# Kernel tuning notes

Hardware: AMD Instinct MI355X
Metric: run time of the kernel (lower is better)

Reference implementation:

```python
import jax, jax.numpy as jnp
import numpy as np

H = W = 1024          # image_shape (square)
ZP, PH, PW = 16, 32, 32   # psf z-stack shape
THRESH = 2.0          # detection_threshold
K = 1024              # spots_per_frame
ROISIZE = PW          # default roisize = psf.shape[-1]
BG_R = PW * 2         # default bg_filter_size
MAXF = PW             # default max_filter_size


def setup_inputs() -> dict:
    key = jax.random.key(0)
    k1, k2 = jax.random.split(key)
    image = jax.random.uniform(k1, (H, W), jnp.float32) * 100.0
    psf = jax.random.uniform(k2, (ZP, PH, PW), jnp.float32)
    psf = psf / jnp.sum(psf, axis=(1, 2), keepdims=True)  # normalized PSF stack
    return {"image": image, "psf": psf}


def _precompute_filters(psf):
    pad = (H - PH) // 2  # square image/psf -> same pad both dims
    psf_padded = jnp.pad(psf, ((0, 0), (pad, pad), (pad, pad)))
    psf_padded = jnp.fft.fftshift(psf_padded, axes=(1, 2))
    psf_fd = jnp.flip(jnp.fft.fft2(psf_padded), axis=(1, 2))
    rr = (jnp.arange(H) - H // 2)[:, None] ** 2 + (jnp.arange(W) - W // 2)[None, :] ** 2
    bg = (rr < BG_R ** 2).astype(jnp.float32) / (np.pi * BG_R ** 2)
    bg_fd = jnp.fft.fft2(jnp.fft.fftshift(bg))
    return psf_fd, bg_fd


def reference(image, psf):
    psf_fd, bg_fd = _precompute_filters(psf)
    image_fd = jnp.fft.fft2(image)
    conv_psf = jnp.fft.ifft2(image_fd[None] * psf_fd).real       # [Z,H,W]
    conv_bg = jnp.fft.ifft2(image_fd * bg_fd).real               # [H,W]
    ratio = conv_psf / (conv_bg[None] + 1.0)                     # matched-filter SNR
    result = ratio.max(axis=0)                                   # [H,W]
    zmap = jnp.argmax(ratio, axis=0)                             # best z plane

    # MaxPool2d(MAXF, stride=1, padding=MAXF//2-1): torch pads with -inf,
    # output is [H-1,W-1]; torch code then zero-pads one row/col at top-left.
    p = MAXF // 2 - 1
    mx = jax.lax.reduce_window(result, -jnp.inf, jax.lax.max,
                               (MAXF, MAXF), (1, 1), ((p, p), (p, p)))
    mx = jnp.pad(mx, ((1, 0), (1, 0)))                           # back to [H,W]

    mask = jnp.where((mx == result) & (result > THRESH), result, 0.0)
    values, indices = jax.lax.top_k(mask.ravel(), K)
    x = indices % W
    y = indices // H  # torch divides by input_shape[0]; square so == W
    roy = y - ROISIZE // 2
    rox = x - ROISIZE // 2
    valid = ((values > THRESH)
             & (roy >= 0) & (roy < H - ROISIZE)
             & (rox >= 0) & (rox < W - ROISIZE))

    # fixed-shape version of boolean select: clamp for safe gather, mask invalids
    roy_c = jnp.clip(roy, 0, H - ROISIZE)
    rox_c = jnp.clip(rox, 0, W - ROISIZE)
    r = jnp.arange(ROISIZE)
    Y = roy_c[:, None, None] + r[None, :, None]                  # [K,R,1]
    X = rox_c[:, None, None] + r[None, None, :]                  # [K,1,R]
    rois = image[Y, X] * valid[:, None, None].astype(image.dtype)  # [K,R,R]

    roipos = jnp.stack((roy_c, rox_c), -1) * valid[:, None]
    intensity = values * valid
    return roipos, intensity, rois, valid
```

## Files before the change

### kernel.cpp

```cpp
#include <hip/hip_runtime.h>
#include <stdint.h>

typedef float v4f __attribute__((ext_vector_type(4)));
typedef int   v8i __attribute__((ext_vector_type(8)));

#define PEX_STRIDE 1156
#define CSTRIDE 858
#define WS_IMG8   0
#define WS_BFRAG  1048576
#define WS_PEX    1064960
#define WS_RESULT 9994240
#define WS_CAND   14188544

__device__ inline unsigned char f32_to_e4m3(float v) {
    if (!(v > 0.0f)) return 0;
    if (v >= 448.0f) return 0x7e;
    if (v < 0.015625f) {
        int m = (int)(v * 512.0f + 0.5f);
        if (m > 7) return 0x08;
        return (unsigned char)m;
    }
    unsigned int u = __float_as_uint(v) + 0x00080000u;
    int e = (int)((u >> 23) & 0xff) - 127;
    int m3 = (int)(u >> 20) & 7;
    int e8 = e + 7;
    if (e8 >= 16) return 0x7e;
    return (unsigned char)((e8 << 3) | m3);
}

__global__ void k_pex(const float* __restrict__ img, float* __restrict__ pex,
                      uint32_t* __restrict__ img8, const float* __restrict__ psf,
                      unsigned char* __restrict__ bf, unsigned int* cnt,
                      float4* __restrict__ out, int n4) {
    __shared__ float wtot[4];
    int blk = blockIdx.x, t = threadIdx.x;
    if (blk >= 1024) {
        if (blk < 2080) {
            int i = (blk - 1024) * 256 + t;
            if (i < n4) { float4 z; z.x = z.y = z.z = z.w = 0.f; out[i] = z; }
        } else {
            int u = (blk - 2080) * 256 + t;
            if (u == 0) cnt[0] = 0u;
            int kb4 = u >> 11; int l = (u >> 5) & 63; int b = u & 31;
            int z = l & 15; int a = kb4 * 4 + (l >> 4);
            float p = psf[z * 1024 + a * 32 + b];
            float c = cosf((float)(a + b - 32) * (6.283185307179586f / 1024.0f));
            bf[u] = f32_to_e4m3(p * c * 1024.0f);
        }
        return;
    }
    int r = blk;
    const float* row = img + r * 1024;
    float s[5];
    float acc = 0.f;
    int base = t * 5;
    #pragma unroll
    for (int j = 0; j < 5; j++) {
        int c = base + j;
        float v = (c < 1152) ? row[(c - 64) & 1023] : 0.f;
        acc += v; s[j] = acc;
    }
    float sc = acc;
    int lane = t & 63, w = t >> 6;
    #pragma unroll
    for (int off = 1; off < 64; off <<= 1) {
        float v = __shfl_up(sc, off, 64);
        if (lane >= off) sc += v;
    }
    if (lane == 63) wtot[w] = sc;
    __syncthreads();
    float wbase = 0.f;
    #pragma unroll
    for (int i = 0; i < 3; i++) if (i < w) wbase += wtot[i];
    float excl = wbase + (sc - acc);
    float* prow = pex + r * PEX_STRIDE;
    if (t == 0) prow[0] = 0.f;
    #pragma unroll
    for (int j = 0; j < 5; j++) {
        int c = base + j;
        if (c < 1152) prow[c + 1] = excl + s[j];
    }
    float4 v4 = *(const float4*)(row + 4 * t);
    img8[r * 256 + t] = (uint32_t)f32_to_e4m3(v4.x)
                      | ((uint32_t)f32_to_e4m3(v4.y) << 8)
                      | ((uint32_t)f32_to_e4m3(v4.z) << 16)
                      | ((uint32_t)f32_to_e4m3(v4.w) << 24);
}

__device__ inline v8i ldsB(const unsigned long long* p) {
    unsigned long long q0 = p[0], q1 = p[1], q2 = p[2], q3 = p[3];
    v8i v;
    v[0] = (int)(unsigned int)q0;  v[1] = (int)(unsigned int)(q0 >> 32);
    v[2] = (int)(unsigned int)q1;  v[3] = (int)(unsigned int)(q1 >> 32);
    v[4] = (int)(unsigned int)q2;  v[5] = (int)(unsigned int)(q2 >> 32);
    v[6] = (int)(unsigned int)q3;  v[7] = (int)(unsigned int)(q3 >> 32);
    return v;
}

__global__ __launch_bounds__(512, 4) void k_conv(
    const unsigned long long* __restrict__ img64,
    const unsigned char* __restrict__ bfrag,
    const float* __restrict__ pex, float* __restrict__ result) {
    __shared__ unsigned long long sm[8 * CSTRIDE];
    __shared__ float rbp[8][5][8];
    __shared__ float rbv[8][5];
    int tid = threadIdx.x;
    int wave = tid >> 6, lane = tid & 63;
    int b = blockIdx.x;
    int tr = b >> 5, tc = b & 31;
    int r0 = tr * 64, c0 = tc * 32;

    for (int u = tid; u < 665; u += 512) {
        int dr = u / 7;
        int x8 = u - dr * 7;
        int row = (r0 + dr - 16) & 1023;
        int cb0 = (c0 + x8 * 8 - 16) & 1023;
        int cb1 = (cb0 + 8) & 1023;
        unsigned long long lo = img64[row * 128 + (cb0 >> 3)];
        unsigned long long hi = img64[row * 128 + (cb1 >> 3)];
        int dst = dr * 9 + x8;
        sm[dst] = lo;
        #pragma unroll
        for (int s = 1; s < 8; s++)
            sm[s * CSTRIDE + dst] = (lo >> (8 * s)) | (hi << (64 - 8 * s));
    }

    if (lane < 40) {
        int si = lane / 5, kc = lane - si * 5;
        int baserow = r0 + si * 8 + 3;
        int n = c0 + 8 * kc;
        int j0 = wave * 16;
        int j1 = j0 + 16; if (j1 > 127) j1 = 127;
        float acc = 0.f;
        for (int j = j0; j < j1; j++) {
            int dy = j - 63;
            int ady = dy < 0 ? -dy : dy;
            int w = (int)sqrtf((float)(4095 - ady * ady));
            const float* p = pex + ((baserow + dy) & 1023) * PEX_STRIDE + n;
            acc += p[65 + w] - p[64 - w];
        }
        rbp[si][kc][wave] = acc;
    }
    __syncthreads();
    if (tid < 40) {
        int si = tid / 5, kc = tid - si * 5;
        float s = 0.f;
        #pragma unroll
        for (int h = 0; h < 8; h++) s += rbp[si][kc][h];
        const float kk = (float)(1.0 / (3.14159265358979323846 * 4096.0));
        rbv[si][kc] = 1.0f / ((s * kk + 1.0f) * 1024.0f);
    }

    int i0 = (wave >> 1) * 16;
    int cw = (wave & 1) * 16;
    int q = lane >> 4;
    int n = lane & 15;
    const unsigned long long* bpq =
        sm + (n & 7) * CSTRIDE + ((cw + n) >> 3) + (i0 + q) * 9;
    const v8i* bfA = (const v8i*)(bfrag + lane * 32);

    float zmax[16];
    #pragma unroll
    for (int h = 0; h < 2; h++) {
        #pragma unroll
        for (int p = 0; p < 4; p++) {
            const unsigned long long* tp = bpq + (h * 8 + p) * 9;
            v4f a0 = (v4f)0.0f, a1 = (v4f)0.0f;
            v8i bcur = ldsB(tp);
            #pragma unroll
            for (int kb4 = 0; kb4 < 8; kb4++) {
                v8i bnxt = ldsB(tp + (4 * (kb4 + 1)) * 9);
                v8i av = bfA[kb4 << 6];
                a0 = __builtin_amdgcn_mfma_scale_f32_16x16x128_f8f6f4(
                        av, bcur, a0, 0, 0, 0, 0x7f7f7f7f, 0, 0x7f7f7f7f);
                a1 = __builtin_amdgcn_mfma_scale_f32_16x16x128_f8f6f4(
                        av, bnxt, a1, 0, 0, 0, 0x7f7f7f7f, 0, 0x7f7f7f7f);
                bcur = bnxt;
            }
            float m0 = fmaxf(fmaxf(a0.x, a0.y), fmaxf(a0.z, a0.w));
            m0 = fmaxf(m0, __shfl_xor(m0, 16, 64));
            m0 = fmaxf(m0, __shfl_xor(m0, 32, 64));
            zmax[h * 8 + p] = m0;
            float m1 = fmaxf(fmaxf(a1.x, a1.y), fmaxf(a1.z, a1.w));
            m1 = fmaxf(m1, __shfl_xor(m1, 16, 64));
            m1 = fmaxf(m1, __shfl_xor(m1, 32, 64));
            zmax[h * 8 + p + 4] = m1;
            __builtin_amdgcn_sched_barrier(0);
        }
    }
    __syncthreads();

    int uu = cw + n;
    int kc = uu >> 3;
    float fr = (float)(uu & 7) * 0.125f;
    int gcol = c0 + uu;
    #pragma unroll
    for (int c4 = 0; c4 < 4; c4++) {
        float m01 = (q & 1) ? zmax[c4 * 4 + 1] : zmax[c4 * 4 + 0];
        float m23 = (q & 1) ? zmax[c4 * 4 + 3] : zmax[c4 * 4 + 2];
        float m = (q & 2) ? m23 : m01;
        int lrow = i0 + c4 * 4 + q;
        int sil = lrow >> 3;
        float rv0 = rbv[sil][kc], rv1 = rbv[sil][kc + 1];
        float rbl = rv0 + fr * (rv1 - rv0);
        result[(r0 + lrow) * 1024 + gcol] = m * rbl;
    }
}

__global__ __launch_bounds__(256) void k_maxcand(const float* __restrict__ result,
                                                 unsigned int* cnt,
                                                 unsigned long long* cand) {
    __shared__ float ls[95 * 96];
    __shared__ float hr[95 * 64];
    __shared__ float wmax[4];
    int bx = blockIdx.x & 15, by = blockIdx.x >> 4;
    int i0 = by * 64, j0 = bx * 64;
    int t = threadIdx.x;
    const float4* cb4 = (const float4*)(result + i0 * 1024 + j0);
    float mx = -3.4e38f;
    #pragma unroll
    for (int k = 0; k < 4; k++) {
        int idx = k * 256 + t;
        float4 v = cb4[(idx >> 4) * 256 + (idx & 15)];
        mx = fmaxf(mx, fmaxf(fmaxf(v.x, v.y), fmaxf(v.z, v.w)));
    }
    #pragma unroll
    for (int m = 1; m < 64; m <<= 1) mx = fmaxf(mx, __shfl_xor(mx, m, 64));
    if ((t & 63) == 0) wmax[t >> 6] = mx;
    __syncthreads();
    float tmax = fmaxf(fmaxf(wmax[0], wmax[1]), fmaxf(wmax[2], wmax[3]));
    if (tmax <= 2.0f) return;

    for (int idx = t; idx < 95 * 95; idx += 256) {
        int r = idx / 95, c = idx - r * 95;
        int gr = i0 - 16 + r, gc = j0 - 16 + c;
        float v = -3.4e38f;
        if ((unsigned)gr < 1024u && (unsigned)gc < 1024u) v = result[gr * 1024 + gc];
        ls[r * 96 + c] = v;
    }
    __syncthreads();
    for (int idx = t; idx < 95 * 64; idx += 256) {
        int r = idx >> 6, c = idx & 63;
        const float* p = ls + r * 96 + c;
        float m = p[0];
        #pragma unroll
        for (int d = 1; d < 32; d++) m = fmaxf(m, p[d]);
        hr[idx] = m;
    }
    __syncthreads();
    for (int idx = t; idx < 64 * 64; idx += 256) {
        int r = idx >> 6, c = idx & 63;
        const float* p = hr + r * 64 + c;
        float m = p[0];
        #pragma unroll
        for (int d = 1; d < 32; d++) m = fmaxf(m, p[d * 64]);
        float v = ls[(r + 16) * 96 + (c + 16)];
        int gi = i0 + r, gj = j0 + c;
        if (gi >= 1 && gj >= 1 && v > 2.0f && v == m) {
            unsigned int k = atomicAdd(cnt, 1u);
            if (k < 2048)
                cand[k] = ((unsigned long long)__float_as_uint(v) << 32)
                        | (unsigned int)(~(unsigned int)(gi * 1024 + gj));
        }
    }
}

__global__ __launch_bounds__(1024) void k_final(
    const float* __restrict__ image, const unsigned int* __restrict__ cnt,
    const unsigned long long* __restrict__ cand, float* __restrict__ out) {
    __shared__ unsigned long long keys[2048];
    int t = threadIdx.x;
    int n = (int)cnt[0]; if (n > 2048) n = 2048;
    if (n == 0) return;
    for (int k = t; k < 2048; k += 1024) keys[k] = (k < n) ? cand[k] : 0ull;
    __syncthreads();
    for (int size = 2; size <= 2048; size <<= 1) {
        for (int stride = size >> 1; stride > 0; stride >>= 1) {
            for (int i = t; i < 2048; i += 1024) {
                int ixj = i ^ stride;
                if (ixj > i) {
                    unsigned long long a = keys[i], b = keys[ixj];
                    bool sw = ((i & size) == 0) ? (a < b) : (a > b);
                    if (sw) { keys[i] = b; keys[ixj] = a; }
                }
            }
            __syncthreads();
        }
    }
    float* roipos = out;
    float* intensity = out + 2048;
    float* rois = out + 3072;
    float* validf = out + 3072 + 1048576;
    int nw = n < 1024 ? n : 1024;
    if (t < nw) {
        unsigned long long key = keys[t];
        float val = __uint_as_float((unsigned int)(key >> 32));
        unsigned int p = ~(unsigned int)key;
        int y = (int)(p >> 10), x = (int)(p & 1023);
        int roy = y - 16, rox = x - 16;
        bool valid = (roy >= 0 && roy < 992 && rox >= 0 && rox < 992);
        int royc = roy < 0 ? 0 : (roy > 992 ? 992 : roy);
        int roxc = rox < 0 ? 0 : (rox > 992 ? 992 : rox);
        roipos[2 * t]     = valid ? (float)royc : 0.f;
        roipos[2 * t + 1] = valid ? (float)roxc : 0.f;
        intensity[t]      = valid ? val : 0.f;
        validf[t]         = valid ? 1.f : 0.f;
    }
    __syncthreads();
    for (int k = 0; k < nw; k++) {
        unsigned long long key = keys[k];
        unsigned int p = ~(unsigned int)key;
        int y = (int)(p >> 10), x = (int)(p & 1023);
        int roy = y - 16, rox = x - 16;
        if (!(roy >= 0 && roy < 992 && rox >= 0 && rox < 992)) continue;
        int u = t >> 5, vv = t & 31;
        rois[k * 1024 + t] = image[(roy + u) * 1024 + (rox + vv)];
    }
}

extern "C" void kernel_launch(void* const* d_in, const int* in_sizes, int n_in,
                              void* d_out, int out_size, void* d_ws, size_t ws_size,
                              hipStream_t stream) {
    const float* image = (const float*)d_in[0];
    const float* psf   = (const float*)d_in[1];
    float* out = (float*)d_out;
    char* ws = (char*)d_ws;
    unsigned char* img8  = (unsigned char*)(ws + WS_IMG8);
    unsigned char* bfrag = (unsigned char*)(ws + WS_BFRAG);
    float* pex = (float*)(ws + WS_PEX);
    float* result = (float*)(ws + WS_RESULT);
    unsigned int* cnt = (unsigned int*)(ws + WS_CAND);
    unsigned long long* cand = (unsigned long long*)(ws + WS_CAND + 16);

    int n4 = out_size / 4;
    hipLaunchKernelGGL(k_pex,     dim3(2144), dim3(256), 0, stream,
                       image, pex, (uint32_t*)img8, psf, bfrag, cnt, (float4*)d_out, n4);
    hipLaunchKernelGGL(k_conv,    dim3(512),  dim3(512), 0, stream,
                       (const unsigned long long*)img8, bfrag, pex, result);
    hipLaunchKernelGGL(k_maxcand, dim3(256),  dim3(256), 0, stream, result, cnt, cand);
    hipLaunchKernelGGL(k_final,   dim3(1),    dim3(1024), 0, stream, image, cnt, cand, out);
}
```

Measured before the change: 96.45 us.

## Halve conv tile height and fuse final sort into maxcand via last-block pattern

The conv kernel now uses 32-row tiles with 256-thread blocks and 1024 blocks instead of 64-row tiles with 512 threads, shrinking shared memory per block and raising the block count. The separate single-block final kernel is merged into the max-filter kernel: each block bumps a second counter after a threadfence, and the last block to finish sorts the candidates and gathers the ROIs with 256 threads. This removes one kernel launch and its gap, but the sort and ROI gather now run on a quarter as many threads, and the smaller conv tiles reload more halo.

```diff
diff --git a/kernel.cpp b/kernel.cpp
--- a/kernel.cpp
+++ b/kernel.cpp
@@ -5,7 +5,7 @@
 typedef int   v8i __attribute__((ext_vector_type(8)));
 
 #define PEX_STRIDE 1156
-#define CSTRIDE 858
+#define CSTRIDE 570
 #define WS_IMG8   0
 #define WS_BFRAG  1048576
 #define WS_PEX    1064960
@@ -40,7 +40,7 @@
             if (i < n4) { float4 z; z.x = z.y = z.z = z.w = 0.f; out[i] = z; }
         } else {
             int u = (blk - 2080) * 256 + t;
-            if (u == 0) cnt[0] = 0u;
+            if (u == 0) { cnt[0] = 0u; cnt[1] = 0u; }
             int kb4 = u >> 11; int l = (u >> 5) & 63; int b = u & 31;
             int z = l & 15; int a = kb4 * 4 + (l >> 4);
             float p = psf[z * 1024 + a * 32 + b];
@@ -97,20 +97,20 @@
     return v;
 }
 
-__global__ __launch_bounds__(512, 4) void k_conv(
+__global__ __launch_bounds__(256, 4) void k_conv(
     const unsigned long long* __restrict__ img64,
     const unsigned char* __restrict__ bfrag,
     const float* __restrict__ pex, float* __restrict__ result) {
     __shared__ unsigned long long sm[8 * CSTRIDE];
-    __shared__ float rbp[8][5][8];
-    __shared__ float rbv[8][5];
+    __shared__ float rbp[4][5][4];
+    __shared__ float rbv[4][5];
     int tid = threadIdx.x;
     int wave = tid >> 6, lane = tid & 63;
     int b = blockIdx.x;
     int tr = b >> 5, tc = b & 31;
-    int r0 = tr * 64, c0 = tc * 32;
-
-    for (int u = tid; u < 665; u += 512) {
+    int r0 = tr * 32, c0 = tc * 32;
+
+    for (int u = tid; u < 441; u += 256) {
         int dr = u / 7;
         int x8 = u - dr * 7;
         int row = (r0 + dr - 16) & 1023;
@@ -125,12 +125,12 @@
             sm[s * CSTRIDE + dst] = (lo >> (8 * s)) | (hi << (64 - 8 * s));
     }
 
-    if (lane < 40) {
+    if (lane < 20) {
         int si = lane / 5, kc = lane - si * 5;
         int baserow = r0 + si * 8 + 3;
         int n = c0 + 8 * kc;
-        int j0 = wave * 16;
-        int j1 = j0 + 16; if (j1 > 127) j1 = 127;
+        int j0 = wave * 32;
+        int j1 = j0 + 32; if (j1 > 127) j1 = 127;
         float acc = 0.f;
         for (int j = j0; j < j1; j++) {
             int dy = j - 63;
@@ -142,11 +142,11 @@
         rbp[si][kc][wave] = acc;
     }
     __syncthreads();
-    if (tid < 40) {
+    if (tid < 20) {
         int si = tid / 5, kc = tid - si * 5;
         float s = 0.f;
         #pragma unroll
-        for (int h = 0; h < 8; h++) s += rbp[si][kc][h];
+        for (int h = 0; h < 4; h++) s += rbp[si][kc][h];
         const float kk = (float)(1.0 / (3.14159265358979323846 * 4096.0));
         rbv[si][kc] = 1.0f / ((s * kk + 1.0f) * 1024.0f);
     }
@@ -207,12 +207,16 @@
     }
 }
 
-__global__ __launch_bounds__(256) void k_maxcand(const float* __restrict__ result,
-                                                 unsigned int* cnt,
-                                                 unsigned long long* cand) {
+__global__ __launch_bounds__(256) void k_maxfin(
+    const float* __restrict__ result, const float* __restrict__ image,
+    unsigned int* cnt, unsigned long long* cand, float* __restrict__ out) {
     __shared__ float ls[95 * 96];
-    __shared__ float hr[95 * 64];
+    __shared__ union {
+        float hr[95 * 64];
+        unsigned long long keys[2048];
+    } ov;
     __shared__ float wmax[4];
+    __shared__ unsigned int lastflag;
     int bx = blockIdx.x & 15, by = blockIdx.x >> 4;
     int i0 = by * 64, j0 = bx * 64;
     int t = threadIdx.x;
@@ -229,59 +233,60 @@
     if ((t & 63) == 0) wmax[t >> 6] = mx;
     __syncthreads();
     float tmax = fmaxf(fmaxf(wmax[0], wmax[1]), fmaxf(wmax[2], wmax[3]));
-    if (tmax <= 2.0f) return;
-
-    for (int idx = t; idx < 95 * 95; idx += 256) {
-        int r = idx / 95, c = idx - r * 95;
-        int gr = i0 - 16 + r, gc = j0 - 16 + c;
-        float v = -3.4e38f;
-        if ((unsigned)gr < 1024u && (unsigned)gc < 1024u) v = result[gr * 1024 + gc];
-        ls[r * 96 + c] = v;
-    }
-    __syncthreads();
-    for (int idx = t; idx < 95 * 64; idx += 256) {
-        int r = idx >> 6, c = idx & 63;
-        const float* p = ls + r * 96 + c;
-        float m = p[0];
-        #pragma unroll
-        for (int d = 1; d < 32; d++) m = fmaxf(m, p[d]);
-        hr[idx] = m;
-    }
-    __syncthreads();
-    for (int idx = t; idx < 64 * 64; idx += 256) {
-        int r = idx >> 6, c = idx & 63;
-        const float* p = hr + r * 64 + c;
-        float m = p[0];
-        #pragma unroll
-        for (int d = 1; d < 32; d++) m = fmaxf(m, p[d * 64]);
-        float v = ls[(r + 16) * 96 + (c + 16)];
-        int gi = i0 + r, gj = j0 + c;
-        if (gi >= 1 && gj >= 1 && v > 2.0f && v == m) {
-            unsigned int k = atomicAdd(cnt, 1u);
-            if (k < 2048)
-                cand[k] = ((unsigned long long)__float_as_uint(v) << 32)
-                        | (unsigned int)(~(unsigned int)(gi * 1024 + gj));
-        }
-    }
-}
-
-__global__ __launch_bounds__(1024) void k_final(
-    const float* __restrict__ image, const unsigned int* __restrict__ cnt,
-    const unsigned long long* __restrict__ cand, float* __restrict__ out) {
-    __shared__ unsigned long long keys[2048];
-    int t = threadIdx.x;
+    if (tmax > 2.0f) {
+        for (int idx = t; idx < 95 * 95; idx += 256) {
+            int r = idx / 95, c = idx - r * 95;
+            int gr = i0 - 16 + r, gc = j0 - 16 + c;
+            float v = -3.4e38f;
+            if ((unsigned)gr < 1024u && (unsigned)gc < 1024u) v = result[gr * 1024 + gc];
+            ls[r * 96 + c] = v;
+        }
+        __syncthreads();
+        for (int idx = t; idx < 95 * 64; idx += 256) {
+            int r = idx >> 6, c = idx & 63;
+            const float* p = ls + r * 96 + c;
+            float m = p[0];
+            #pragma unroll
+            for (int d = 1; d < 32; d++) m = fmaxf(m, p[d]);
+            ov.hr[idx] = m;
+        }
+        __syncthreads();
+        for (int idx = t; idx < 64 * 64; idx += 256) {
+            int r = idx >> 6, c = idx & 63;
+            const float* p = ov.hr + r * 64 + c;
+            float m = p[0];
+            #pragma unroll
+            for (int d = 1; d < 32; d++) m = fmaxf(m, p[d * 64]);
+            float v = ls[(r + 16) * 96 + (c + 16)];
+            int gi = i0 + r, gj = j0 + c;
+            if (gi >= 1 && gj >= 1 && v > 2.0f && v == m) {
+                unsigned int k = atomicAdd(cnt, 1u);
+                if (k < 2048)
+                    cand[k] = ((unsigned long long)__float_as_uint(v) << 32)
+                            | (unsigned int)(~(unsigned int)(gi * 1024 + gj));
+            }
+        }
+    }
+    __threadfence();
+    __syncthreads();
+    if (t == 0) lastflag = (atomicAdd(&cnt[1], 1u) == 255u) ? 1u : 0u;
+    __syncthreads();
+    if (lastflag == 0u) return;
+    __threadfence();
+
     int n = (int)cnt[0]; if (n > 2048) n = 2048;
     if (n == 0) return;
-    for (int k = t; k < 2048; k += 1024) keys[k] = (k < n) ? cand[k] : 0ull;
+    __syncthreads();
+    for (int k = t; k < 2048; k += 256) ov.keys[k] = (k < n) ? cand[k] : 0ull;
     __syncthreads();
     for (int size = 2; size <= 2048; size <<= 1) {
         for (int stride = size >> 1; stride > 0; stride >>= 1) {
-            for (int i = t; i < 2048; i += 1024) {
+            for (int i = t; i < 2048; i += 256) {
                 int ixj = i ^ stride;
                 if (ixj > i) {
-                    unsigned long long a = keys[i], b = keys[ixj];
+                    unsigned long long a = ov.keys[i], b = ov.keys[ixj];
                     bool sw = ((i & size) == 0) ? (a < b) : (a > b);
-                    if (sw) { keys[i] = b; keys[ixj] = a; }
+                    if (sw) { ov.keys[i] = b; ov.keys[ixj] = a; }
                 }
             }
             __syncthreads();
@@ -292,8 +297,8 @@
     float* rois = out + 3072;
     float* validf = out + 3072 + 1048576;
     int nw = n < 1024 ? n : 1024;
-    if (t < nw) {
-        unsigned long long key = keys[t];
+    for (int tt = t; tt < nw; tt += 256) {
+        unsigned long long key = ov.keys[tt];
         float val = __uint_as_float((unsigned int)(key >> 32));
         unsigned int p = ~(unsigned int)key;
         int y = (int)(p >> 10), x = (int)(p & 1023);
@@ -301,20 +306,24 @@
         bool valid = (roy >= 0 && roy < 992 && rox >= 0 && rox < 992);
         int royc = roy < 0 ? 0 : (roy > 992 ? 992 : roy);
         int roxc = rox < 0 ? 0 : (rox > 992 ? 992 : rox);
-        roipos[2 * t]     = valid ? (float)royc : 0.f;
-        roipos[2 * t + 1] = valid ? (float)roxc : 0.f;
-        intensity[t]      = valid ? val : 0.f;
-        validf[t]         = valid ? 1.f : 0.f;
+        roipos[2 * tt]     = valid ? (float)royc : 0.f;
+        roipos[2 * tt + 1] = valid ? (float)roxc : 0.f;
+        intensity[tt]      = valid ? val : 0.f;
+        validf[tt]         = valid ? 1.f : 0.f;
     }
     __syncthreads();
     for (int k = 0; k < nw; k++) {
-        unsigned long long key = keys[k];
+        unsigned long long key = ov.keys[k];
         unsigned int p = ~(unsigned int)key;
         int y = (int)(p >> 10), x = (int)(p & 1023);
         int roy = y - 16, rox = x - 16;
         if (!(roy >= 0 && roy < 992 && rox >= 0 && rox < 992)) continue;
-        int u = t >> 5, vv = t & 31;
-        rois[k * 1024 + t] = image[(roy + u) * 1024 + (rox + vv)];
+        #pragma unroll
+        for (int m = 0; m < 4; m++) {
+            int idx = t + 256 * m;
+            int u = idx >> 5, vv = idx & 31;
+            rois[k * 1024 + idx] = image[(roy + u) * 1024 + (rox + vv)];
+        }
     }
 }
 
@@ -333,10 +342,10 @@
     unsigned long long* cand = (unsigned long long*)(ws + WS_CAND + 16);
 
     int n4 = out_size / 4;
-    hipLaunchKernelGGL(k_pex,     dim3(2144), dim3(256), 0, stream,
+    hipLaunchKernelGGL(k_pex,    dim3(2144), dim3(256), 0, stream,
                        image, pex, (uint32_t*)img8, psf, bfrag, cnt, (float4*)d_out, n4);
-    hipLaunchKernelGGL(k_conv,    dim3(512),  dim3(512), 0, stream,
+    hipLaunchKernelGGL(k_conv,   dim3(1024), dim3(256), 0, stream,
                        (const unsigned long long*)img8, bfrag, pex, result);
-    hipLaunchKernelGGL(k_maxcand, dim3(256),  dim3(256), 0, stream, result, cnt, cand);
-    hipLaunchKernelGGL(k_final,   dim3(1),    dim3(1024), 0, stream, image, cnt, cand, out);
-}
+    hipLaunchKernelGGL(k_maxfin, dim3(256),  dim3(256), 0, stream,
+                       result, image, cnt, cand, out);
+}
```

Result: slower. 117.1 us (+21.4%).
